# Optimization experiments

Hardware: AMD Instinct MI355X
Metric: run time of the kernel (lower is better)

Reference implementation:

```python
import jax, jax.numpy as jnp
import numpy as np

B, S1, S2 = 16, 256, 512          # batch, vision len, text len
V_HID, T_HID = 1024, 768          # v_hidden_size, hidden_size
BI_HID, H = 1024, 8               # bi_hidden_size, bi_num_attention_heads
D = BI_HID // H                   # attention_head_size = 128


def setup_inputs() -> dict:
    key = jax.random.key(0)
    ks = jax.random.split(key, 16)
    s = 0.02
    inp = {
        "input_tensor1": jax.random.normal(ks[0], (B, S1, V_HID), jnp.float32),
        "attention_mask1": jnp.zeros((B, 1, 1, S1), jnp.float32),
        "input_tensor2": jax.random.normal(ks[1], (B, S2, T_HID), jnp.float32),
        "attention_mask2": jnp.zeros((B, 1, 1, S2), jnp.float32),
        # vision-stream projections (query1/key1/value1): v_hidden -> all_head_size
        "Wq1": jax.random.normal(ks[2], (V_HID, BI_HID), jnp.float32) * s,
        "bq1": jnp.zeros((BI_HID,), jnp.float32),
        "Wk1": jax.random.normal(ks[3], (V_HID, BI_HID), jnp.float32) * s,
        "bk1": jnp.zeros((BI_HID,), jnp.float32),
        "Wv1": jax.random.normal(ks[4], (V_HID, BI_HID), jnp.float32) * s,
        "bv1": jnp.zeros((BI_HID,), jnp.float32),
        # text-stream projections (query2/key2/value2): hidden -> all_head_size
        "Wq2": jax.random.normal(ks[5], (T_HID, BI_HID), jnp.float32) * s,
        "bq2": jnp.zeros((BI_HID,), jnp.float32),
        "Wk2": jax.random.normal(ks[6], (T_HID, BI_HID), jnp.float32) * s,
        "bk2": jnp.zeros((BI_HID,), jnp.float32),
        "Wv2": jax.random.normal(ks[7], (T_HID, BI_HID), jnp.float32) * s,
        "bv2": jnp.zeros((BI_HID,), jnp.float32),
    }
    return inp


def _heads(x):
    # [B, S, H*D] -> [B, S, H, D]
    b, s, _ = x.shape
    return x.reshape(b, s, H, D)


def reference(input_tensor1, attention_mask1, input_tensor2, attention_mask2,
              Wq1, bq1, Wk1, bk1, Wv1, bv1,
              Wq2, bq2, Wk2, bk2, Wv2, bv2):
    scale = 1.0 / jnp.sqrt(jnp.asarray(D, input_tensor1.dtype))
    # stream 1 (vision) QKV
    q1 = _heads(input_tensor1 @ Wq1 + bq1)
    k1 = _heads(input_tensor1 @ Wk1 + bk1)
    v1 = _heads(input_tensor1 @ Wv1 + bv1)
    # stream 2 (text) QKV
    q2 = _heads(input_tensor2 @ Wq2 + bq2)
    k2 = _heads(input_tensor2 @ Wk2 + bk2)
    v2 = _heads(input_tensor2 @ Wv2 + bv2)

    # attention 1: text queries attend to vision keys/values  -> context1 [B,S2,BI_HID]
    scores1 = jnp.einsum('bqhd,bkhd->bhqk', q2, k1) * scale + attention_mask1
    probs1 = jax.nn.softmax(scores1, axis=-1)  # dropout prob = 0 (eval)
    context1 = jnp.einsum('bhqk,bkhd->bqhd', probs1, v1).reshape(B, S2, BI_HID)

    # attention 2: vision queries attend to text keys/values  -> context2 [B,S1,BI_HID]
    scores2 = jnp.einsum('bqhd,bkhd->bhqk', q1, k2) * scale + attention_mask2
    probs2 = jax.nn.softmax(scores2, axis=-1)
    context2 = jnp.einsum('bhqk,bkhd->bqhd', probs2, v2).reshape(B, S1, BI_HID)

    return (context1, context2)
```

## Files before the change

### kernel.cpp

```cpp
#include <hip/hip_runtime.h>


typedef _Float16 f16;
typedef unsigned int u32;
typedef f16  v8h __attribute__((ext_vector_type(8)));
typedef float v4f __attribute__((ext_vector_type(4)));

struct alignas(8) h4 { f16 x, y, z, w; };

#define GLL16(g, l) __builtin_amdgcn_global_load_lds(                          \
    (const __attribute__((address_space(1))) u32*)(g),                         \
    (__attribute__((address_space(3))) u32*)(l), 16, 0, 0)

#define MFMA16 __builtin_amdgcn_mfma_f32_16x16x32_f16

__global__ __launch_bounds__(256)
void cvt_in(const float* __restrict__ p1, long n1,
            const float* __restrict__ p2, long n2,
            f16* __restrict__ d1, f16* __restrict__ d2)
{
    long i = ((long)blockIdx.x * 256 + threadIdx.x) * 8;
    const float* s; f16* d;
    if (i < n1) { s = p1 + i; d = d1 + i; }
    else        { long j = i - n1; if (j >= n2) return; s = p2 + j; d = d2 + j; }
    float4 a = *(const float4*)s, b = *(const float4*)(s + 4);
    v8h o = {(f16)a.x, (f16)a.y, (f16)a.z, (f16)a.w,
             (f16)b.x, (f16)b.y, (f16)b.z, (f16)b.w};
    *(v8h*)d = o;
}

__global__ __launch_bounds__(256)
void cvt_wT(const float* __restrict__ w0, const float* __restrict__ w1,
            const float* __restrict__ w2, const float* __restrict__ w3,
            const float* __restrict__ w4, const float* __restrict__ w5,
            f16* __restrict__ o1, f16* __restrict__ o2)
{
    const int z = blockIdx.z;
    const int K = z < 3 ? 1024 : 768;
    const int bk = blockIdx.y * 64;
    if (bk >= K) return;
    const float* src = z == 0 ? w0 : z == 1 ? w1 : z == 2 ? w2
                     : z == 3 ? w3 : z == 4 ? w4 : w5;
    f16* dst = z < 3 ? o1 + (size_t)z * 1024 * 1024
                     : o2 + (size_t)(z - 3) * 1024 * 768;

    __shared__ float t[64][65];
    const int bn = blockIdx.x * 64;
    const int r0 = threadIdx.x >> 4, c4 = (threadIdx.x & 15) * 4;
#pragma unroll
    for (int rr = 0; rr < 64; rr += 16) {
        float4 v = *(const float4*)&src[(long)(bk + rr + r0) * 1024 + bn + c4];
        t[rr + r0][c4 + 0] = v.x; t[rr + r0][c4 + 1] = v.y;
        t[rr + r0][c4 + 2] = v.z; t[rr + r0][c4 + 3] = v.w;
    }
    __syncthreads();
#pragma unroll
    for (int rr = 0; rr < 64; rr += 16) {
        const int n = rr + r0;
        h4 o = {(f16)t[c4 + 0][n], (f16)t[c4 + 1][n],
                (f16)t[c4 + 2][n], (f16)t[c4 + 3][n]};
        *(h4*)&dst[(long)(bn + n) * K + bk + c4] = o;
    }
}

__global__ __launch_bounds__(256, 3)
void mm_proj(const f16* __restrict__ A, const f16* __restrict__ Bw,
             const float* __restrict__ bq, const float* __restrict__ bk,
             const float* __restrict__ bv,
             f16* __restrict__ qo, f16* __restrict__ ko, f16* __restrict__ vo,
             int K, int S)
{
    __shared__ f16 sh[17408];
    f16* As = sh;
    f16* Bs = sh + 4096;
    const int m0 = blockIdx.y * 128, n0 = blockIdx.x * 128;
    const int tid = threadIdx.x, lane = tid & 63, w = tid >> 6;
    const int wm = w >> 1, wn = w & 1;
    const int fr = lane & 15, fq = lane >> 4;

    int aoff[4], boff[4];
#pragma unroll
    for (int t = 0; t < 4; ++t) {
        const int ra = wm * 64 + t * 16 + fr;
        aoff[t] = ra * 32 + (fq ^ ((ra >> 1) & 3)) * 8;
        const int rb = wn * 64 + t * 16 + fr;
        boff[t] = rb * 32 + (fq ^ ((rb >> 1) & 3)) * 8;
    }

    v4f acc[4][4];
#pragma unroll
    for (int i = 0; i < 4; ++i)
#pragma unroll
        for (int j = 0; j < 4; ++j) acc[i][j] = (v4f){0.f, 0.f, 0.f, 0.f};

    for (int k0 = 0; k0 < K; k0 += 32) {
#pragma unroll
        for (int j = 0; j < 2; ++j) {
            const int c = j * 256 + tid, row = c >> 2;
            const int kl = (c & 3) ^ ((row >> 1) & 3);
            GLL16(A + (long)(m0 + row) * K + k0 + kl * 8, As + c * 8);
        }
#pragma unroll
        for (int j = 0; j < 2; ++j) {
            const int c = j * 256 + tid, row = c >> 2;
            const int kl = (c & 3) ^ ((row >> 1) & 3);
            GLL16(Bw + (long)(n0 + row) * K + k0 + kl * 8, Bs + c * 8);
        }
        __syncthreads();

        v8h ah[4], bh[4];
#pragma unroll
        for (int t = 0; t < 4; ++t) ah[t] = *(const v8h*)&As[aoff[t]];
#pragma unroll
        for (int t = 0; t < 4; ++t) bh[t] = *(const v8h*)&Bs[boff[t]];
#pragma unroll
        for (int tmi = 0; tmi < 4; ++tmi)
#pragma unroll
            for (int tni = 0; tni < 4; ++tni)
                acc[tmi][tni] = MFMA16(ah[tmi], bh[tni], acc[tmi][tni], 0, 0, 0);
        __syncthreads();
    }

    const int col = lane & 15, quad = lane >> 4;
    const int seg = n0 >> 10, nbase = n0 & 1023;
    f16* buf = sh;

    if (seg < 2) {
        const float* bias = seg == 0 ? bq : bk;
#pragma unroll
        for (int tmi = 0; tmi < 4; ++tmi) {
            const int ml = wm * 64 + tmi * 16 + quad * 4;
#pragma unroll
            for (int tni = 0; tni < 4; ++tni) {
                const int nl = wn * 64 + tni * 16 + col;
                const float bvl = bias[nbase + nl];
#pragma unroll
                for (int i = 0; i < 4; ++i)
                    buf[(ml + i) * 136 + nl] = (f16)(acc[tmi][tni][i] + bvl);
            }
        }
        __syncthreads();
        f16* Co = seg == 0 ? qo : ko;
        const int rr = tid >> 1, hf = tid & 1;
        const long gb = (long)(m0 + rr) * 1024 + nbase + hf * 64;
#pragma unroll
        for (int c = 0; c < 8; ++c)
            *(v8h*)&Co[gb + c * 8] = *(const v8h*)&buf[rr * 136 + hf * 64 + c * 8];
    } else {
#pragma unroll
        for (int tmi = 0; tmi < 4; ++tmi) {
            const int ml = wm * 64 + tmi * 16 + quad * 4;
#pragma unroll
            for (int tni = 0; tni < 4; ++tni) {
                const int nl = wn * 64 + tni * 16 + col;
                const float bvl = bv[nbase + nl];
                h4 o = {(f16)(acc[tmi][tni][0] + bvl), (f16)(acc[tmi][tni][1] + bvl),
                        (f16)(acc[tmi][tni][2] + bvl), (f16)(acc[tmi][tni][3] + bvl)};
                *(h4*)&buf[nl * 136 + ml] = o;
            }
        }
        __syncthreads();
        const int bb = m0 / S, s0 = m0 % S;
        const int nn = tid >> 1, hf = tid & 1;
        const long gb = ((long)bb * 1024 + nbase + nn) * S + s0 + hf * 64;
#pragma unroll
        for (int c = 0; c < 8; ++c)
            *(v8h*)&vo[gb + c * 8] = *(const v8h*)&buf[nn * 136 + hf * 64 + c * 8];
    }
}

template<int RT>
__global__ __launch_bounds__(256, RT == 1 ? 3 : 2)
void flash(const f16* __restrict__ qp, const f16* __restrict__ kp,
           const f16* __restrict__ vp, const float* __restrict__ mask,
           float* __restrict__ out, int Sq, int Sk, float scale)
{
    constexpr int PSTR = 72;
    __shared__ f16 lds[16384 + RT * 64 * PSTR];
    f16* KL = lds;
    f16* VL = lds + 8192;
    f16* PL = lds + 16384;
    f16* QL = lds;

    const int b = blockIdx.z >> 3, hd = blockIdx.z & 7;
    const int q0 = blockIdx.y * (RT * 64);
    const int tid = threadIdx.x, lane = tid & 63, w = tid >> 6;
    const int col = lane & 15, quad = lane >> 4;

    const long qoff = ((long)b * Sq + q0) * 1024 + (long)hd * 128;
#pragma unroll
    for (int j = 0; j < RT * 4; ++j) {
        const int c = j * 256 + tid, row = c >> 4, ch = (c & 15) ^ (row & 15);
        GLL16(qp + qoff + (long)row * 1024 + ch * 8, QL + c * 8);
    }
    __syncthreads();
    v8h qf[RT][4];
#pragma unroll
    for (int rt = 0; rt < RT; ++rt) {
        const int row = w * (RT * 16) + rt * 16 + col;
#pragma unroll
        for (int kf = 0; kf < 4; ++kf)
            qf[rt][kf] = *(const v8h*)&QL[row * 128 + ((kf * 4 + quad) ^ (row & 15)) * 8];
    }

    v8h ones;
#pragma unroll
    for (int i = 0; i < 8; ++i) ones[i] = (f16)1.0f;

    v4f O[RT][8], Lc[RT];
#pragma unroll
    for (int rt = 0; rt < RT; ++rt) {
#pragma unroll
        for (int nj = 0; nj < 8; ++nj) O[rt][nj] = (v4f){0.f, 0.f, 0.f, 0.f};
        Lc[rt] = (v4f){0.f, 0.f, 0.f, 0.f};
    }

    const long kbase = (long)b * Sk * 1024 + (long)hd * 128;
    const long vbase = ((long)b * 1024 + hd * 128) * (long)Sk;

    for (int kt = 0; kt < (Sk >> 6); ++kt) {
        __syncthreads();
#pragma unroll
        for (int j = 0; j < 4; ++j) {
            const int c = j * 256 + tid, row = c >> 4, ch = (c & 15) ^ (row & 15);
            GLL16(kp + kbase + (long)(kt * 64 + row) * 1024 + ch * 8, KL + c * 8);
        }
#pragma unroll
        for (int j = 0; j < 4; ++j) {
            const int c = j * 256 + tid, row = c >> 3, ch = (c & 7) ^ (row & 7);
            GLL16(vp + vbase + (long)row * Sk + kt * 64 + ch * 8, VL + c * 8);
        }
        __syncthreads();

        v4f sa[RT][4];
#pragma unroll
        for (int rt = 0; rt < RT; ++rt)
#pragma unroll
            for (int tn = 0; tn < 4; ++tn) sa[rt][tn] = (v4f){0.f, 0.f, 0.f, 0.f};
#pragma unroll
        for (int kf = 0; kf < 4; ++kf) {
            v8h bh[4];
#pragma unroll
            for (int tn = 0; tn < 4; ++tn) {
                const int row = tn * 16 + col;
                bh[tn] = *(const v8h*)&KL[row * 128 + ((kf * 4 + quad) ^ (row & 15)) * 8];
            }
#pragma unroll
            for (int rt = 0; rt < RT; ++rt)
#pragma unroll
                for (int tn = 0; tn < 4; ++tn)
                    sa[rt][tn] = MFMA16(qf[rt][kf], bh[tn], sa[rt][tn], 0, 0, 0);
        }

        float mv[4];
#pragma unroll
        for (int tn = 0; tn < 4; ++tn)
            mv[tn] = mask[(long)b * Sk + kt * 64 + tn * 16 + col];
#pragma unroll
        for (int rt = 0; rt < RT; ++rt)
#pragma unroll
            for (int tn = 0; tn < 4; ++tn)
#pragma unroll
                for (int r = 0; r < 4; ++r) {
                    const float p = __expf(sa[rt][tn][r] * scale + mv[tn]);
                    PL[(w * RT * 16 + rt * 16 + quad * 4 + r) * PSTR + tn * 16 + col]
                        = (f16)p;
                }

#pragma unroll
        for (int kf2 = 0; kf2 < 2; ++kf2) {
            v8h vb[8];
#pragma unroll
            for (int nj = 0; nj < 8; ++nj) {
                const int row = nj * 16 + col;
                vb[nj] = *(const v8h*)&VL[row * 64 + ((kf2 * 4 + quad) ^ (row & 7)) * 8];
            }
#pragma unroll
            for (int rt = 0; rt < RT; ++rt) {
                const v8h pa = *(const v8h*)&PL[(w * RT * 16 + rt * 16 + col) * PSTR
                                                + kf2 * 32 + quad * 8];
#pragma unroll
                for (int nj = 0; nj < 8; ++nj)
                    O[rt][nj] = MFMA16(pa, vb[nj], O[rt][nj], 0, 0, 0);
                Lc[rt] = MFMA16(pa, ones, Lc[rt], 0, 0, 0);
            }
        }
    }

#pragma unroll
    for (int rt = 0; rt < RT; ++rt) {
        float inv[4];
#pragma unroll
        for (int r = 0; r < 4; ++r) inv[r] = 1.0f / Lc[rt][r];
        const long ob = ((long)b * Sq + q0 + w * (RT * 16) + rt * 16 + quad * 4) * 1024
                        + (long)hd * 128;
#pragma unroll
        for (int nj = 0; nj < 8; ++nj)
#pragma unroll
            for (int r = 0; r < 4; ++r)
                out[ob + (long)r * 1024 + nj * 16 + col] = O[rt][nj][r] * inv[r];
    }
}

extern "C" void kernel_launch(void* const* d_in, const int* in_sizes, int n_in,
                              void* d_out, int out_size, void* d_ws, size_t ws_size,
                              hipStream_t stream)
{
    const float* in1   = (const float*)d_in[0];
    const float* mask1 = (const float*)d_in[1];
    const float* in2   = (const float*)d_in[2];
    const float* mask2 = (const float*)d_in[3];
    const float* Wq1 = (const float*)d_in[4];  const float* bq1 = (const float*)d_in[5];
    const float* Wk1 = (const float*)d_in[6];  const float* bk1 = (const float*)d_in[7];
    const float* Wv1 = (const float*)d_in[8];  const float* bv1 = (const float*)d_in[9];
    const float* Wq2 = (const float*)d_in[10]; const float* bq2 = (const float*)d_in[11];
    const float* Wk2 = (const float*)d_in[12]; const float* bk2 = (const float*)d_in[13];
    const float* Wv2 = (const float*)d_in[14]; const float* bv2 = (const float*)d_in[15];

    constexpr int Bb = 16, S1 = 256, S2 = 512, VH = 1024, TH = 768;
    constexpr long M1 = (long)Bb * S1, M2 = (long)Bb * S2;
    const float scale = 0.088388347648318447f;

    f16* W = (f16*)d_ws;
    f16* i1  = W;
    f16* i2  = i1 + M1 * VH;
    f16* w1  = i2 + M2 * TH;
    f16* w2  = w1 + (long)3072 * VH;
    f16* q1  = w2 + (long)3072 * TH;
    f16* k1  = q1 + M1 * 1024;
    f16* v1t = k1 + M1 * 1024;
    f16* q2  = v1t + M1 * 1024;
    f16* k2  = q2 + M2 * 1024;
    f16* v2t = k2 + M2 * 1024;
    float* out = (float*)d_out;

    cvt_in<<<dim3(5120), 256, 0, stream>>>(in1, M1 * VH, in2, M2 * TH, i1, i2);
    cvt_wT<<<dim3(16, 16, 6), 256, 0, stream>>>(Wq1, Wk1, Wv1, Wq2, Wk2, Wv2, w1, w2);

    mm_proj<<<dim3(24, 32), 256, 0, stream>>>(i1, w1, bq1, bk1, bv1,
                                              q1, k1, v1t, VH, S1);
    mm_proj<<<dim3(24, 64), 256, 0, stream>>>(i2, w2, bq2, bk2, bv2,
                                              q2, k2, v2t, TH, S2);

    flash<2><<<dim3(1, 4, 128), 256, 0, stream>>>(q2, k1, v1t, mask1,
                                                  out, S2, S1, scale);
    flash<1><<<dim3(1, 4, 128), 256, 0, stream>>>(q1, k2, v2t, mask2,
                                                  out + M2 * 1024, S1, S2, scale);
}
```

Before: 289.6 us.

## Double GEMM K-step, remap block order for L2 locality, raise occupancy bounds

```diff
diff --git a/kernel.cpp b/kernel.cpp
--- a/kernel.cpp
+++ b/kernel.cpp
@@ -63,61 +63,66 @@
     }
 }
 
-__global__ __launch_bounds__(256, 3)
+__global__ __launch_bounds__(256, 4)
 void mm_proj(const f16* __restrict__ A, const f16* __restrict__ Bw,
              const float* __restrict__ bq, const float* __restrict__ bk,
              const float* __restrict__ bv,
              f16* __restrict__ qo, f16* __restrict__ ko, f16* __restrict__ vo,
-             int K, int S)
+             int K, int S, int mdiv)
 {
     __shared__ f16 sh[17408];
     f16* As = sh;
-    f16* Bs = sh + 4096;
-    const int m0 = blockIdx.y * 128, n0 = blockIdx.x * 128;
+    f16* Bs = sh + 8192;
+
+    const int id = blockIdx.x + 24 * blockIdx.y;
+    const int by = (id & 7) * mdiv + ((id >> 3) % mdiv);
+    const int bx = id / (8 * mdiv);
+    const int m0 = by * 128, n0 = bx * 128;
+
     const int tid = threadIdx.x, lane = tid & 63, w = tid >> 6;
     const int wm = w >> 1, wn = w & 1;
     const int fr = lane & 15, fq = lane >> 4;
 
-    int aoff[4], boff[4];
-#pragma unroll
-    for (int t = 0; t < 4; ++t) {
-        const int ra = wm * 64 + t * 16 + fr;
-        aoff[t] = ra * 32 + (fq ^ ((ra >> 1) & 3)) * 8;
-        const int rb = wn * 64 + t * 16 + fr;
-        boff[t] = rb * 32 + (fq ^ ((rb >> 1) & 3)) * 8;
-    }
-
     v4f acc[4][4];
 #pragma unroll
     for (int i = 0; i < 4; ++i)
 #pragma unroll
         for (int j = 0; j < 4; ++j) acc[i][j] = (v4f){0.f, 0.f, 0.f, 0.f};
 
-    for (int k0 = 0; k0 < K; k0 += 32) {
-#pragma unroll
-        for (int j = 0; j < 2; ++j) {
-            const int c = j * 256 + tid, row = c >> 2;
-            const int kl = (c & 3) ^ ((row >> 1) & 3);
+    for (int k0 = 0; k0 < K; k0 += 64) {
+#pragma unroll
+        for (int j = 0; j < 4; ++j) {
+            const int c = j * 256 + tid, row = c >> 3;
+            const int kl = (c & 7) ^ (row & 7);
             GLL16(A + (long)(m0 + row) * K + k0 + kl * 8, As + c * 8);
         }
 #pragma unroll
-        for (int j = 0; j < 2; ++j) {
-            const int c = j * 256 + tid, row = c >> 2;
-            const int kl = (c & 3) ^ ((row >> 1) & 3);
+        for (int j = 0; j < 4; ++j) {
+            const int c = j * 256 + tid, row = c >> 3;
+            const int kl = (c & 7) ^ (row & 7);
             GLL16(Bw + (long)(n0 + row) * K + k0 + kl * 8, Bs + c * 8);
         }
         __syncthreads();
 
-        v8h ah[4], bh[4];
-#pragma unroll
-        for (int t = 0; t < 4; ++t) ah[t] = *(const v8h*)&As[aoff[t]];
-#pragma unroll
-        for (int t = 0; t < 4; ++t) bh[t] = *(const v8h*)&Bs[boff[t]];
-#pragma unroll
-        for (int tmi = 0; tmi < 4; ++tmi)
-#pragma unroll
-            for (int tni = 0; tni < 4; ++tni)
-                acc[tmi][tni] = MFMA16(ah[tmi], bh[tni], acc[tmi][tni], 0, 0, 0);
+#pragma unroll
+        for (int s = 0; s < 2; ++s) {
+            v8h ah[4], bh[4];
+#pragma unroll
+            for (int t = 0; t < 4; ++t) {
+                const int ra = wm * 64 + t * 16 + fr;
+                ah[t] = *(const v8h*)&As[ra * 64 + ((s * 4 + fq) ^ (ra & 7)) * 8];
+            }
+#pragma unroll
+            for (int t = 0; t < 4; ++t) {
+                const int rb = wn * 64 + t * 16 + fr;
+                bh[t] = *(const v8h*)&Bs[rb * 64 + ((s * 4 + fq) ^ (rb & 7)) * 8];
+            }
+#pragma unroll
+            for (int tmi = 0; tmi < 4; ++tmi)
+#pragma unroll
+                for (int tni = 0; tni < 4; ++tni)
+                    acc[tmi][tni] = MFMA16(ah[tmi], bh[tni], acc[tmi][tni], 0, 0, 0);
+        }
         __syncthreads();
     }
 
@@ -170,7 +175,7 @@
 }
 
 template<int RT>
-__global__ __launch_bounds__(256, RT == 1 ? 3 : 2)
+__global__ __launch_bounds__(256, 3)
 void flash(const f16* __restrict__ qp, const f16* __restrict__ kp,
            const f16* __restrict__ vp, const float* __restrict__ mask,
            float* __restrict__ out, int Sq, int Sk, float scale)
@@ -182,8 +187,10 @@
     f16* PL = lds + 16384;
     f16* QL = lds;
 
-    const int b = blockIdx.z >> 3, hd = blockIdx.z & 7;
-    const int q0 = blockIdx.y * (RT * 64);
+    const int lid = blockIdx.y + 4 * blockIdx.z;
+    const int zz = lid & 127, yy = lid >> 7;
+    const int b = zz >> 3, hd = zz & 7;
+    const int q0 = yy * (RT * 64);
     const int tid = threadIdx.x, lane = tid & 63, w = tid >> 6;
     const int col = lane & 15, quad = lane >> 4;
 
@@ -338,9 +345,9 @@
     cvt_wT<<<dim3(16, 16, 6), 256, 0, stream>>>(Wq1, Wk1, Wv1, Wq2, Wk2, Wv2, w1, w2);
 
     mm_proj<<<dim3(24, 32), 256, 0, stream>>>(i1, w1, bq1, bk1, bv1,
-                                              q1, k1, v1t, VH, S1);
+                                              q1, k1, v1t, VH, S1, 4);
     mm_proj<<<dim3(24, 64), 256, 0, stream>>>(i2, w2, bq2, bk2, bv2,
-                                              q2, k2, v2t, TH, S2);
+                                              q2, k2, v2t, TH, S2, 8);
 
     flash<2><<<dim3(1, 4, 128), 256, 0, stream>>>(q2, k1, v1t, mask1,
                                                   out, S2, S1, scale);
```

Result: faster. 272.9 us (-5.8%).

## Merge stream launches, double-buffer GEMM LDS, and unify flash tiles

Applied to the files above, without the earlier changes.

```diff
diff --git a/kernel.cpp b/kernel.cpp
--- a/kernel.cpp
+++ b/kernel.cpp
@@ -63,17 +63,31 @@
     }
 }
 
-__global__ __launch_bounds__(256, 3)
-void mm_proj(const f16* __restrict__ A, const f16* __restrict__ Bw,
-             const float* __restrict__ bq, const float* __restrict__ bk,
-             const float* __restrict__ bv,
-             f16* __restrict__ qo, f16* __restrict__ ko, f16* __restrict__ vo,
-             int K, int S)
-{
-    __shared__ f16 sh[17408];
-    f16* As = sh;
-    f16* Bs = sh + 4096;
-    const int m0 = blockIdx.y * 128, n0 = blockIdx.x * 128;
+__global__ __launch_bounds__(256, 4)
+void mm_proj(const f16* __restrict__ A2, const f16* __restrict__ B2,
+             const float* __restrict__ bq2, const float* __restrict__ bk2,
+             const float* __restrict__ bv2,
+             f16* __restrict__ q2o, f16* __restrict__ k2o, f16* __restrict__ v2o,
+             const f16* __restrict__ A1, const f16* __restrict__ B1,
+             const float* __restrict__ bq1, const float* __restrict__ bk1,
+             const float* __restrict__ bv1,
+             f16* __restrict__ q1o, f16* __restrict__ k1o, f16* __restrict__ v1o)
+{
+    __shared__ f16 sh[16384];
+
+    const int gid = blockIdx.x;
+    const bool is2 = gid < 1536;
+    const int id   = is2 ? gid : gid - 1536;
+    const int K    = is2 ? 768 : 1024;
+    const int S    = is2 ? 512 : 256;
+    const int mdiv = is2 ? 8 : 4;
+    const f16* A  = is2 ? A2 : A1;
+    const f16* Bw = is2 ? B2 : B1;
+
+    const int by = (id & 7) * mdiv + ((id >> 3) % mdiv);
+    const int bx = id / (8 * mdiv);
+    const int m0 = by * 128, n0 = bx * 128;
+
     const int tid = threadIdx.x, lane = tid & 63, w = tid >> 6;
     const int wm = w >> 1, wn = w & 1;
     const int fr = lane & 15, fq = lane >> 4;
@@ -82,32 +96,36 @@
 #pragma unroll
     for (int t = 0; t < 4; ++t) {
         const int ra = wm * 64 + t * 16 + fr;
-        aoff[t] = ra * 32 + (fq ^ ((ra >> 1) & 3)) * 8;
+        aoff[t] = ra * 32 + (fq ^ (ra & 3)) * 8;
         const int rb = wn * 64 + t * 16 + fr;
-        boff[t] = rb * 32 + (fq ^ ((rb >> 1) & 3)) * 8;
-    }
-
-    v4f acc[4][4];
-#pragma unroll
-    for (int i = 0; i < 4; ++i)
-#pragma unroll
-        for (int j = 0; j < 4; ++j) acc[i][j] = (v4f){0.f, 0.f, 0.f, 0.f};
-
-    for (int k0 = 0; k0 < K; k0 += 32) {
+        boff[t] = rb * 32 + (fq ^ (rb & 3)) * 8;
+    }
+
+    auto stage = [&](int k0, int p) {
+        f16* Ad = sh + p * 4096;
+        f16* Bd = sh + 8192 + p * 4096;
 #pragma unroll
         for (int j = 0; j < 2; ++j) {
             const int c = j * 256 + tid, row = c >> 2;
-            const int kl = (c & 3) ^ ((row >> 1) & 3);
-            GLL16(A + (long)(m0 + row) * K + k0 + kl * 8, As + c * 8);
-        }
-#pragma unroll
-        for (int j = 0; j < 2; ++j) {
-            const int c = j * 256 + tid, row = c >> 2;
-            const int kl = (c & 3) ^ ((row >> 1) & 3);
-            GLL16(Bw + (long)(n0 + row) * K + k0 + kl * 8, Bs + c * 8);
-        }
+            const int kl = (c & 3) ^ (row & 3);
+            GLL16(A  + (long)(m0 + row) * K + k0 + kl * 8, Ad + c * 8);
+            GLL16(Bw + (long)(n0 + row) * K + k0 + kl * 8, Bd + c * 8);
+        }
+    };
+
+    v4f acc[4][4];
+#pragma unroll
+    for (int i = 0; i < 4; ++i)
+#pragma unroll
+        for (int j = 0; j < 4; ++j) acc[i][j] = (v4f){0.f, 0.f, 0.f, 0.f};
+
+    stage(0, 0);
+    const int NK = K >> 5;
+    for (int kt = 0; kt < NK; ++kt) {
         __syncthreads();
-
+        if (kt + 1 < NK) stage((kt + 1) << 5, (kt + 1) & 1);
+        const f16* As = sh + (kt & 1) * 4096;
+        const f16* Bs = sh + 8192 + (kt & 1) * 4096;
         v8h ah[4], bh[4];
 #pragma unroll
         for (int t = 0; t < 4; ++t) ah[t] = *(const v8h*)&As[aoff[t]];
@@ -118,7 +136,6 @@
 #pragma unroll
             for (int tni = 0; tni < 4; ++tni)
                 acc[tmi][tni] = MFMA16(ah[tmi], bh[tni], acc[tmi][tni], 0, 0, 0);
-        __syncthreads();
     }
 
     const int col = lane & 15, quad = lane >> 4;
@@ -126,94 +143,119 @@
     f16* buf = sh;
 
     if (seg < 2) {
-        const float* bias = seg == 0 ? bq : bk;
-#pragma unroll
-        for (int tmi = 0; tmi < 4; ++tmi) {
-            const int ml = wm * 64 + tmi * 16 + quad * 4;
-#pragma unroll
-            for (int tni = 0; tni < 4; ++tni) {
-                const int nl = wn * 64 + tni * 16 + col;
-                const float bvl = bias[nbase + nl];
-#pragma unroll
-                for (int i = 0; i < 4; ++i)
-                    buf[(ml + i) * 136 + nl] = (f16)(acc[tmi][tni][i] + bvl);
-            }
-        }
-        __syncthreads();
-        f16* Co = seg == 0 ? qo : ko;
-        const int rr = tid >> 1, hf = tid & 1;
-        const long gb = (long)(m0 + rr) * 1024 + nbase + hf * 64;
-#pragma unroll
-        for (int c = 0; c < 8; ++c)
-            *(v8h*)&Co[gb + c * 8] = *(const v8h*)&buf[rr * 136 + hf * 64 + c * 8];
+        const float* bias = seg == 0 ? (is2 ? bq2 : bq1) : (is2 ? bk2 : bk1);
+        f16* Co = seg == 0 ? (is2 ? q2o : q1o) : (is2 ? k2o : k1o);
+#pragma unroll
+        for (int pass = 0; pass < 2; ++pass) {
+            __syncthreads();
+            if (wm == pass) {
+#pragma unroll
+                for (int tmi = 0; tmi < 4; ++tmi) {
+                    const int ml = tmi * 16 + quad * 4;
+#pragma unroll
+                    for (int tni = 0; tni < 4; ++tni) {
+                        const int nl = wn * 64 + tni * 16 + col;
+                        const float bvl = bias[nbase + nl];
+#pragma unroll
+                        for (int i = 0; i < 4; ++i)
+                            buf[(ml + i) * 136 + nl] = (f16)(acc[tmi][tni][i] + bvl);
+                    }
+                }
+            }
+            __syncthreads();
+            const int rr = tid >> 2, cc = (tid & 3) * 32;
+            const long gb = (long)(m0 + pass * 64 + rr) * 1024 + nbase + cc;
+#pragma unroll
+            for (int c = 0; c < 4; ++c)
+                *(v8h*)&Co[gb + c * 8] = *(const v8h*)&buf[rr * 136 + cc + c * 8];
+        }
     } else {
-#pragma unroll
-        for (int tmi = 0; tmi < 4; ++tmi) {
-            const int ml = wm * 64 + tmi * 16 + quad * 4;
-#pragma unroll
-            for (int tni = 0; tni < 4; ++tni) {
-                const int nl = wn * 64 + tni * 16 + col;
-                const float bvl = bv[nbase + nl];
-                h4 o = {(f16)(acc[tmi][tni][0] + bvl), (f16)(acc[tmi][tni][1] + bvl),
-                        (f16)(acc[tmi][tni][2] + bvl), (f16)(acc[tmi][tni][3] + bvl)};
-                *(h4*)&buf[nl * 136 + ml] = o;
-            }
-        }
-        __syncthreads();
+        const float* bias = is2 ? bv2 : bv1;
+        f16* vo = is2 ? v2o : v1o;
         const int bb = m0 / S, s0 = m0 % S;
-        const int nn = tid >> 1, hf = tid & 1;
-        const long gb = ((long)bb * 1024 + nbase + nn) * S + s0 + hf * 64;
-#pragma unroll
-        for (int c = 0; c < 8; ++c)
-            *(v8h*)&vo[gb + c * 8] = *(const v8h*)&buf[nn * 136 + hf * 64 + c * 8];
-    }
-}
-
-template<int RT>
-__global__ __launch_bounds__(256, RT == 1 ? 3 : 2)
-void flash(const f16* __restrict__ qp, const f16* __restrict__ kp,
-           const f16* __restrict__ vp, const float* __restrict__ mask,
-           float* __restrict__ out, int Sq, int Sk, float scale)
+#pragma unroll
+        for (int pass = 0; pass < 2; ++pass) {
+            __syncthreads();
+            if (wn == pass) {
+#pragma unroll
+                for (int tmi = 0; tmi < 4; ++tmi) {
+                    const int ml = wm * 64 + tmi * 16 + quad * 4;
+#pragma unroll
+                    for (int tni = 0; tni < 4; ++tni) {
+                        const int nl = tni * 16 + col;
+                        const float bvl = bias[nbase + pass * 64 + nl];
+                        h4 o = {(f16)(acc[tmi][tni][0] + bvl),
+                                (f16)(acc[tmi][tni][1] + bvl),
+                                (f16)(acc[tmi][tni][2] + bvl),
+                                (f16)(acc[tmi][tni][3] + bvl)};
+                        *(h4*)&buf[nl * 136 + ml] = o;
+                    }
+                }
+            }
+            __syncthreads();
+            const int nn = tid >> 2, mm = (tid & 3) * 32;
+            const long gb = ((long)bb * 1024 + nbase + pass * 64 + nn) * S + s0 + mm;
+#pragma unroll
+            for (int c = 0; c < 4; ++c)
+                *(v8h*)&vo[gb + c * 8] = *(const v8h*)&buf[nn * 136 + mm + c * 8];
+        }
+    }
+}
+
+__global__ __launch_bounds__(256, 3)
+void flash(const f16* __restrict__ q2, const f16* __restrict__ k1,
+           const f16* __restrict__ v1, const float* __restrict__ m1,
+           float* __restrict__ o1,
+           const f16* __restrict__ q1, const f16* __restrict__ k2,
+           const f16* __restrict__ v2, const float* __restrict__ m2,
+           float* __restrict__ o2, float scale)
 {
     constexpr int PSTR = 72;
-    __shared__ f16 lds[16384 + RT * 64 * PSTR];
+    __shared__ f16 lds[16384 + 64 * PSTR];
     f16* KL = lds;
     f16* VL = lds + 8192;
     f16* PL = lds + 16384;
     f16* QL = lds;
 
-    const int b = blockIdx.z >> 3, hd = blockIdx.z & 7;
-    const int q0 = blockIdx.y * (RT * 64);
+    const int gid = blockIdx.x;
+    const bool ph1 = gid < 1024;
+    const int id = ph1 ? gid : gid - 1024;
+    const int Sq = ph1 ? 512 : 256, Sk = ph1 ? 256 : 512;
+    const f16* qp = ph1 ? q2 : q1;
+    const f16* kp = ph1 ? k1 : k2;
+    const f16* vp = ph1 ? v1 : v2;
+    const float* mask = ph1 ? m1 : m2;
+    float* out = ph1 ? o1 : o2;
+
+    const int zz = id & 127, yy = id >> 7;
+    const int b = zz >> 3, hd = zz & 7;
+    const int q0 = yy * 64;
     const int tid = threadIdx.x, lane = tid & 63, w = tid >> 6;
     const int col = lane & 15, quad = lane >> 4;
 
     const long qoff = ((long)b * Sq + q0) * 1024 + (long)hd * 128;
 #pragma unroll
-    for (int j = 0; j < RT * 4; ++j) {
+    for (int j = 0; j < 4; ++j) {
         const int c = j * 256 + tid, row = c >> 4, ch = (c & 15) ^ (row & 15);
         GLL16(qp + qoff + (long)row * 1024 + ch * 8, QL + c * 8);
     }
     __syncthreads();
-    v8h qf[RT][4];
-#pragma unroll
-    for (int rt = 0; rt < RT; ++rt) {
-        const int row = w * (RT * 16) + rt * 16 + col;
+    v8h qf[4];
+    {
+        const int row = w * 16 + col;
 #pragma unroll
         for (int kf = 0; kf < 4; ++kf)
-            qf[rt][kf] = *(const v8h*)&QL[row * 128 + ((kf * 4 + quad) ^ (row & 15)) * 8];
+            qf[kf] = *(const v8h*)&QL[row * 128 + ((kf * 4 + quad) ^ (row & 15)) * 8];
     }
 
     v8h ones;
 #pragma unroll
     for (int i = 0; i < 8; ++i) ones[i] = (f16)1.0f;
 
-    v4f O[RT][8], Lc[RT];
-#pragma unroll
-    for (int rt = 0; rt < RT; ++rt) {
-#pragma unroll
-        for (int nj = 0; nj < 8; ++nj) O[rt][nj] = (v4f){0.f, 0.f, 0.f, 0.f};
-        Lc[rt] = (v4f){0.f, 0.f, 0.f, 0.f};
-    }
+    v4f O[8], Lc;
+#pragma unroll
+    for (int nj = 0; nj < 8; ++nj) O[nj] = (v4f){0.f, 0.f, 0.f, 0.f};
+    Lc = (v4f){0.f, 0.f, 0.f, 0.f};
 
     const long kbase = (long)b * Sk * 1024 + (long)hd * 128;
     const long vbase = ((long)b * 1024 + hd * 128) * (long)Sk;
@@ -232,11 +274,9 @@
         }
         __syncthreads();
 
-        v4f sa[RT][4];
-#pragma unroll
-        for (int rt = 0; rt < RT; ++rt)
-#pragma unroll
-            for (int tn = 0; tn < 4; ++tn) sa[rt][tn] = (v4f){0.f, 0.f, 0.f, 0.f};
+        v4f sa[4];
+#pragma unroll
+        for (int tn = 0; tn < 4; ++tn) sa[tn] = (v4f){0.f, 0.f, 0.f, 0.f};
 #pragma unroll
         for (int kf = 0; kf < 4; ++kf) {
             v8h bh[4];
@@ -246,10 +286,8 @@
                 bh[tn] = *(const v8h*)&KL[row * 128 + ((kf * 4 + quad) ^ (row & 15)) * 8];
             }
 #pragma unroll
-            for (int rt = 0; rt < RT; ++rt)
-#pragma unroll
-                for (int tn = 0; tn < 4; ++tn)
-                    sa[rt][tn] = MFMA16(qf[rt][kf], bh[tn], sa[rt][tn], 0, 0, 0);
+            for (int tn = 0; tn < 4; ++tn)
+                sa[tn] = MFMA16(qf[kf], bh[tn], sa[tn], 0, 0, 0);
         }
 
         float mv[4];
@@ -257,15 +295,12 @@
         for (int tn = 0; tn < 4; ++tn)
             mv[tn] = mask[(long)b * Sk + kt * 64 + tn * 16 + col];
 #pragma unroll
-        for (int rt = 0; rt < RT; ++rt)
-#pragma unroll
-            for (int tn = 0; tn < 4; ++tn)
-#pragma unroll
-                for (int r = 0; r < 4; ++r) {
-                    const float p = __expf(sa[rt][tn][r] * scale + mv[tn]);
-                    PL[(w * RT * 16 + rt * 16 + quad * 4 + r) * PSTR + tn * 16 + col]
-                        = (f16)p;
-                }
+        for (int tn = 0; tn < 4; ++tn)
+#pragma unroll
+            for (int r = 0; r < 4; ++r) {
+                const float p = __expf(sa[tn][r] * scale + mv[tn]);
+                PL[(w * 16 + quad * 4 + r) * PSTR + tn * 16 + col] = (f16)p;
+            }
 
 #pragma unroll
         for (int kf2 = 0; kf2 < 2; ++kf2) {
@@ -275,31 +310,23 @@
                 const int row = nj * 16 + col;
                 vb[nj] = *(const v8h*)&VL[row * 64 + ((kf2 * 4 + quad) ^ (row & 7)) * 8];
             }
-#pragma unroll
-            for (int rt = 0; rt < RT; ++rt) {
-                const v8h pa = *(const v8h*)&PL[(w * RT * 16 + rt * 16 + col) * PSTR
-                                                + kf2 * 32 + quad * 8];
-#pragma unroll
-                for (int nj = 0; nj < 8; ++nj)
-                    O[rt][nj] = MFMA16(pa, vb[nj], O[rt][nj], 0, 0, 0);
-                Lc[rt] = MFMA16(pa, ones, Lc[rt], 0, 0, 0);
-            }
-        }
-    }
-
-#pragma unroll
-    for (int rt = 0; rt < RT; ++rt) {
-        float inv[4];
-#pragma unroll
-        for (int r = 0; r < 4; ++r) inv[r] = 1.0f / Lc[rt][r];
-        const long ob = ((long)b * Sq + q0 + w * (RT * 16) + rt * 16 + quad * 4) * 1024
-                        + (long)hd * 128;
-#pragma unroll
-        for (int nj = 0; nj < 8; ++nj)
-#pragma unroll
-            for (int r = 0; r < 4; ++r)
-                out[ob + (long)r * 1024 + nj * 16 + col] = O[rt][nj][r] * inv[r];
-    }
+            const v8h pa = *(const v8h*)&PL[(w * 16 + col) * PSTR + kf2 * 32 + quad * 8];
+#pragma unroll
+            for (int nj = 0; nj < 8; ++nj)
+                O[nj] = MFMA16(pa, vb[nj], O[nj], 0, 0, 0);
+            Lc = MFMA16(pa, ones, Lc, 0, 0, 0);
+        }
+    }
+
+    float inv[4];
+#pragma unroll
+    for (int r = 0; r < 4; ++r) inv[r] = 1.0f / Lc[r];
+    const long ob = ((long)b * Sq + q0 + w * 16 + quad * 4) * 1024 + (long)hd * 128;
+#pragma unroll
+    for (int nj = 0; nj < 8; ++nj)
+#pragma unroll
+        for (int r = 0; r < 4; ++r)
+            out[ob + (long)r * 1024 + nj * 16 + col] = O[nj][r] * inv[r];
 }
 
 extern "C" void kernel_launch(void* const* d_in, const int* in_sizes, int n_in,
@@ -337,13 +364,11 @@
     cvt_in<<<dim3(5120), 256, 0, stream>>>(in1, M1 * VH, in2, M2 * TH, i1, i2);
     cvt_wT<<<dim3(16, 16, 6), 256, 0, stream>>>(Wq1, Wk1, Wv1, Wq2, Wk2, Wv2, w1, w2);
 
-    mm_proj<<<dim3(24, 32), 256, 0, stream>>>(i1, w1, bq1, bk1, bv1,
-                                              q1, k1, v1t, VH, S1);
-    mm_proj<<<dim3(24, 64), 256, 0, stream>>>(i2, w2, bq2, bk2, bv2,
-                                              q2, k2, v2t, TH, S2);
-
-    flash<2><<<dim3(1, 4, 128), 256, 0, stream>>>(q2, k1, v1t, mask1,
-                                                  out, S2, S1, scale);
-    flash<1><<<dim3(1, 4, 128), 256, 0, stream>>>(q1, k2, v2t, mask2,
-                                                  out + M2 * 1024, S1, S2, scale);
-}
+    mm_proj<<<dim3(2304), 256, 0, stream>>>(
+        i2, w2, bq2, bk2, bv2, q2, k2, v2t,
+        i1, w1, bq1, bk1, bv1, q1, k1, v1t);
+
+    flash<<<dim3(1536), 256, 0, stream>>>(
+        q2, k1, v1t, mask1, out,
+        q1, k2, v2t, mask2, out + M2 * 1024, scale);
+}
```

Result: faster. 262.4 us (-9.4%).
